# Optimization experiments

Measured on AMD Instinct MI355X. Metric: run time of the kernel, lower is better.

Reference implementation:

```python
import jax, jax.numpy as jnp
import numpy as np

B, C, H, W = 8, 512, 96, 96
CQ = 64  # inter_ch


def setup_inputs() -> dict:
    key = jax.random.key(0)
    ks = jax.random.split(key, 8)
    scale = 1.0 / np.sqrt(C)
    return {
        "x": jax.random.normal(ks[0], (B, C, H, W), dtype=jnp.float32),
        "Wq": jax.random.normal(ks[1], (CQ, C), dtype=jnp.float32) * scale,
        "bq": jax.random.normal(ks[2], (CQ,), dtype=jnp.float32) * 0.01,
        "Wk": jax.random.normal(ks[3], (CQ, C), dtype=jnp.float32) * scale,
        "bk": jax.random.normal(ks[4], (CQ,), dtype=jnp.float32) * 0.01,
        "Wv": jax.random.normal(ks[5], (C, C), dtype=jnp.float32) * scale,
        "bv": jax.random.normal(ks[6], (C,), dtype=jnp.float32) * 0.01,
        "gamma": jax.random.normal(ks[7], (1,), dtype=jnp.float32) * 0.1,
    }


def reference(x, Wq, bq, Wk, bk, Wv, bv, gamma):
    # 1x1 convs expressed as channel matmuls; outputs in BHWC layout
    Q = jnp.einsum('bchw,oc->bhwo', x, Wq) + bq   # [B,H,W,CQ]
    K = jnp.einsum('bchw,oc->bhwo', x, Wk) + bk   # [B,H,W,CQ]
    V = jnp.einsum('bchw,oc->bhwo', x, Wv) + bv   # [B,H,W,C]

    # Per pixel (i,j): keys = concat(row i keys [W], column j keys [H]).
    # NOTE: this replication includes pixel (i,j) twice (once in row, once in col),
    # matching the torch loop exactly (no -INF masking as in original CCNet).
    e_row = jnp.einsum('bhwc,bhvc->bhwv', Q, K)   # [B,H,W,W] attend along row h
    e_col = jnp.einsum('bhwc,bgwc->bhwg', Q, K)   # [B,H,W,H] attend along col w
    attn = jax.nn.softmax(jnp.concatenate([e_row, e_col], axis=-1), axis=-1)
    a_row, a_col = attn[..., :W], attn[..., W:]   # [B,H,W,W], [B,H,W,H]

    out = (jnp.einsum('bhwv,bhvc->bhwc', a_row, V)
           + jnp.einsum('bhwg,bgwc->bhwc', a_col, V))  # [B,H,W,C]
    out = jnp.transpose(out, (0, 3, 1, 2))        # [B,C,H,W]
    return x + gamma[0] * out
```

## Files before the change

### kernel.cpp

```cpp
#include <hip/hip_runtime.h>
#include <stdint.h>

#define B_  8
#define C_  512
#define H_  96
#define W_  96
#define CQ_ 64
#define P_  (H_*W_)
#define NP  (B_*P_)
#define L_  (W_+H_)

typedef __attribute__((ext_vector_type(8))) short short8;
typedef __attribute__((ext_vector_type(4))) float f32x4;
typedef __attribute__((ext_vector_type(4))) unsigned short us4;

__device__ __forceinline__ ushort f2bf(float f) {
    uint32_t u = __builtin_bit_cast(uint32_t, f);
    u += 0x7fff + ((u >> 16) & 1);
    return (ushort)(u >> 16);
}
__device__ __forceinline__ float bf2f(ushort h) {
    uint32_t u = ((uint32_t)h) << 16;
    return __builtin_bit_cast(float, u);
}

#define GLL16(g, l) __builtin_amdgcn_global_load_lds( \
    (const __attribute__((address_space(1))) uint32_t*)(g), \
    (__attribute__((address_space(3))) uint32_t*)(l), 16, 0, 0)

#define FSW(r) (((r) >> 1) & 3)

__global__ __launch_bounds__(256) void k_xt(const float* __restrict__ x, ushort* __restrict__ xt) {
    __shared__ float tile[64][65];
    int p0 = blockIdx.x * 64, c0 = blockIdx.y * 64, bat = blockIdx.z;
    int tx = threadIdx.x, ty = threadIdx.y;
    const float* xb = x + ((size_t)bat * C_ + c0) * P_ + p0;
    #pragma unroll
    for (int i = ty; i < 64; i += 8) {
        float2 v = *(const float2*)&xb[(size_t)i * P_ + 2 * tx];
        tile[i][2 * tx] = v.x; tile[i][2 * tx + 1] = v.y;
    }
    __syncthreads();
    ushort* o = xt + ((size_t)bat * P_ + p0) * C_ + c0;
    #pragma unroll
    for (int i = ty; i < 64; i += 8) {
        ushort2 v; v.x = f2bf(tile[2 * tx][i]); v.y = f2bf(tile[2 * tx + 1][i]);
        *(ushort2*)&o[(size_t)i * C_ + 2 * tx] = v;
    }
}

__global__ __launch_bounds__(256) void k_wconv(const float* __restrict__ Wq, const float* __restrict__ Wk,
                                               const float* __restrict__ Wv, const float* __restrict__ bq,
                                               const float* __restrict__ bk, const float* __restrict__ bv,
                                               ushort* __restrict__ Wall, float* __restrict__ ball) {
    int idx = blockIdx.x * 256 + threadIdx.x;
    if (idx < 640) {
        float b;
        if (idx < 64)       b = bq[idx];
        else if (idx < 128) b = bk[idx - 64];
        else                b = bv[idx - 128];
        ball[idx] = b;
    }
    if (idx >= 640 * C_) return;
    int o = idx / C_, c = idx % C_;
    float v;
    if (o < 64)       v = Wq[o * C_ + c];
    else if (o < 128) v = Wk[(o - 64) * C_ + c];
    else              v = Wv[(o - 128) * C_ + c];
    Wall[idx] = f2bf(v);
}

__global__ __launch_bounds__(256, 4) void k_proj(const ushort* __restrict__ xt, const ushort* __restrict__ Wall,
                                                 const float* __restrict__ ball,
                                                 ushort* __restrict__ Qcm, ushort* __restrict__ Kcm,
                                                 ushort* __restrict__ Vcm) {
    __shared__ __align__(16) ushort Al[128 * 32];
    __shared__ __align__(16) ushort Bl[128 * 32];
    int tid = threadIdx.x, lane = tid & 63, wv = tid >> 6;
    int wr = wv >> 1, wc = wv & 1;
    int wg = ((int)blockIdx.x & 7) * 360 + ((int)blockIdx.x >> 3);
    int m0 = (wg % 5) * 128;
    int n0 = (wg / 5) * 128;
    f32x4 acc[4][4] = {};
    for (int kb = 0; kb < C_; kb += 32) {
        #pragma unroll
        for (int i = 0; i < 2; ++i) {
            int u = tid + i * 256, row = u >> 2, seg = u & 3;
            int sg = (seg ^ FSW(row)) << 3;
            GLL16(&Wall[(size_t)(m0 + row) * C_ + kb + sg], &Al[(size_t)u * 8]);
            GLL16(&xt[(size_t)(n0 + row) * C_ + kb + sg],   &Bl[(size_t)u * 8]);
        }
        __syncthreads();
        int rr = lane & 15, gq = lane >> 4, ck = gq ^ FSW(rr);
        short8 fb[4];
        #pragma unroll
        for (int nt = 0; nt < 4; ++nt) fb[nt] = *(const short8*)&Bl[(wc * 64 + nt * 16 + rr) * 32 + ck * 8];
        #pragma unroll
        for (int mt = 0; mt < 4; ++mt) {
            short8 fa = *(const short8*)&Al[(wr * 64 + mt * 16 + rr) * 32 + ck * 8];
            #pragma unroll
            for (int nt = 0; nt < 4; ++nt)
                acc[mt][nt] = __builtin_amdgcn_mfma_f32_16x16x32_bf16(fa, fb[nt], acc[mt][nt], 0, 0, 0);
        }
        __syncthreads();
    }
    int rr = lane & 15, gq = lane >> 4;
    int bat = n0 / P_, pb0 = n0 - bat * P_;
    #pragma unroll
    for (int mt = 0; mt < 4; ++mt)
        #pragma unroll
        for (int nt = 0; nt < 4; ++nt) {
            int col = wc * 64 + nt * 16 + rr;
            #pragma unroll
            for (int q = 0; q < 4; ++q) {
                int o = m0 + wr * 64 + mt * 16 + gq * 4 + q;
                float v = acc[mt][nt][q] + ball[o];
                if (o < 64)       Qcm[(size_t)o * NP + n0 + col] = f2bf(v);
                else if (o < 128) Kcm[(size_t)(o - 64) * NP + n0 + col] = f2bf(v);
                else              Vcm[((size_t)bat * C_ + (o - 128)) * P_ + pb0 + col] = f2bf(v);
            }
        }
}

__global__ __launch_bounds__(256) void k_qkt(const ushort* __restrict__ Qcm, const ushort* __restrict__ Kcm,
                                             ushort* __restrict__ Qb, ushort* __restrict__ Kb) {
    __shared__ ushort t[64][65];
    int p0 = blockIdx.x * 64;
    const ushort* src = blockIdx.y ? Kcm : Qcm;
    ushort* dst = blockIdx.y ? Kb : Qb;
    int tx = threadIdx.x, ty = threadIdx.y;
    #pragma unroll
    for (int i = ty; i < 64; i += 4) t[i][tx] = src[(size_t)i * NP + p0 + tx];
    __syncthreads();
    #pragma unroll
    for (int i = ty; i < 64; i += 4) dst[(size_t)(p0 + i) * CQ_ + tx] = t[tx][i];
}

__global__ __launch_bounds__(256) void k_vt(const ushort* __restrict__ Vcm, ushort* __restrict__ Vt) {
    __shared__ ushort t[96 * 98];
    int c = blockIdx.x, bat = blockIdx.y;
    const ushort* src = Vcm + ((size_t)(bat * C_ + c)) * P_;
    int tid = threadIdx.x;
    for (int u = tid; u < 2304; u += 256) {
        int h = u / 24, w4 = (u % 24) * 4;
        us4 v = *(const us4*)&src[h * 96 + w4];
        ushort2 a; a.x = v.x; a.y = v.y;
        ushort2 b; b.x = v.z; b.y = v.w;
        *(ushort2*)&t[h * 98 + w4]     = a;
        *(ushort2*)&t[h * 98 + w4 + 2] = b;
    }
    __syncthreads();
    for (int u = tid; u < 2304; u += 256) {
        int w = u / 24, h4 = (u % 24) * 4;
        us4 o;
        o.x = t[(h4 + 0) * 98 + w];
        o.y = t[(h4 + 1) * 98 + w];
        o.z = t[(h4 + 2) * 98 + w];
        o.w = t[(h4 + 3) * 98 + w];
        *(us4*)&Vt[((size_t)(bat * W_ + w) * C_ + c) * H_ + h4] = o;
    }
}

#define LSTR 40
__global__ __launch_bounds__(256) void k_erow(const ushort* __restrict__ Qb, const ushort* __restrict__ Kb,
                                              float* __restrict__ logits) {
    __shared__ __align__(16) ushort Al[96 * LSTR];
    __shared__ __align__(16) ushort Bl[96 * LSTR];
    int h = blockIdx.x, bat = blockIdx.y;
    int tid = threadIdx.x, lane = tid & 63, wvid = tid >> 6;
    int wr = wvid >> 1, wc = wvid & 1;
    size_t base = ((size_t)bat * H_ + h) * W_;
    f32x4 acc[3][3] = {};
    for (int kb = 0; kb < CQ_; kb += 32) {
        for (int s = tid; s < 96 * 4; s += 256) {
            int row = s >> 2, seg = s & 3;
            *(short8*)&Al[row * LSTR + seg * 8] = *(const short8*)&Qb[(base + row) * CQ_ + kb + seg * 8];
            *(short8*)&Bl[row * LSTR + seg * 8] = *(const short8*)&Kb[(base + row) * CQ_ + kb + seg * 8];
        }
        __syncthreads();
        int rr = lane & 15, gq = lane >> 4;
        #pragma unroll
        for (int mt = 0; mt < 3; ++mt) {
            short8 fa = *(const short8*)&Al[(wr * 48 + mt * 16 + rr) * LSTR + gq * 8];
            #pragma unroll
            for (int nt = 0; nt < 3; ++nt) {
                short8 fb = *(const short8*)&Bl[(wc * 48 + nt * 16 + rr) * LSTR + gq * 8];
                acc[mt][nt] = __builtin_amdgcn_mfma_f32_16x16x32_bf16(fa, fb, acc[mt][nt], 0, 0, 0);
            }
        }
        __syncthreads();
    }
    int rr = lane & 15, gq = lane >> 4;
    #pragma unroll
    for (int mt = 0; mt < 3; ++mt)
        #pragma unroll
        for (int nt = 0; nt < 3; ++nt)
            #pragma unroll
            for (int q = 0; q < 4; ++q) {
                int w = wr * 48 + mt * 16 + gq * 4 + q;
                int v = wc * 48 + nt * 16 + rr;
                logits[(base + w) * L_ + v] = acc[mt][nt][q];
            }
}

__global__ __launch_bounds__(256) void k_ecol(const ushort* __restrict__ Qb, const ushort* __restrict__ Kb,
                                              float* __restrict__ logits) {
    __shared__ __align__(16) ushort Al[96 * LSTR];
    __shared__ __align__(16) ushort Bl[96 * LSTR];
    int w = blockIdx.x, bat = blockIdx.y;
    int tid = threadIdx.x, lane = tid & 63, wvid = tid >> 6;
    int wr = wvid >> 1, wc = wvid & 1;
    f32x4 acc[3][3] = {};
    for (int kb = 0; kb < CQ_; kb += 32) {
        for (int s = tid; s < 96 * 4; s += 256) {
            int row = s >> 2, seg = s & 3;
            size_t px = ((size_t)bat * H_ + row) * W_ + w;
            *(short8*)&Al[row * LSTR + seg * 8] = *(const short8*)&Qb[px * CQ_ + kb + seg * 8];
            *(short8*)&Bl[row * LSTR + seg * 8] = *(const short8*)&Kb[px * CQ_ + kb + seg * 8];
        }
        __syncthreads();
        int rr = lane & 15, gq = lane >> 4;
        #pragma unroll
        for (int mt = 0; mt < 3; ++mt) {
            short8 fa = *(const short8*)&Al[(wr * 48 + mt * 16 + rr) * LSTR + gq * 8];
            #pragma unroll
            for (int nt = 0; nt < 3; ++nt) {
                short8 fb = *(const short8*)&Bl[(wc * 48 + nt * 16 + rr) * LSTR + gq * 8];
                acc[mt][nt] = __builtin_amdgcn_mfma_f32_16x16x32_bf16(fa, fb, acc[mt][nt], 0, 0, 0);
            }
        }
        __syncthreads();
    }
    int rr = lane & 15, gq = lane >> 4;
    #pragma unroll
    for (int mt = 0; mt < 3; ++mt)
        #pragma unroll
        for (int nt = 0; nt < 3; ++nt)
            #pragma unroll
            for (int q = 0; q < 4; ++q) {
                int hh = wr * 48 + mt * 16 + gq * 4 + q;
                int gg = wc * 48 + nt * 16 + rr;
                logits[(((size_t)bat * H_ + hh) * W_ + w) * L_ + W_ + gg] = acc[mt][nt][q];
            }
}

__global__ __launch_bounds__(256) void k_softmax(const float* __restrict__ logits, ushort* __restrict__ attn) {
    int wvid = threadIdx.x >> 6, lane = threadIdx.x & 63;
    size_t px = (size_t)blockIdx.x * 4 + wvid;
    const float* lp = logits + px * L_;
    float v0 = lp[lane], v1 = lp[lane + 64], v2 = lp[lane + 128];
    float m = fmaxf(fmaxf(v0, v1), v2);
    #pragma unroll
    for (int off = 32; off; off >>= 1) m = fmaxf(m, __shfl_xor(m, off));
    float e0 = __expf(v0 - m), e1 = __expf(v1 - m), e2 = __expf(v2 - m);
    float s = e0 + e1 + e2;
    #pragma unroll
    for (int off = 32; off; off >>= 1) s += __shfl_xor(s, off);
    float inv = 1.0f / s;
    ushort* ap = attn + px * L_;
    ap[lane] = f2bf(e0 * inv); ap[lane + 64] = f2bf(e1 * inv); ap[lane + 128] = f2bf(e2 * inv);
}

__global__ __launch_bounds__(512) void k_pvcol(const ushort* __restrict__ Vt, const ushort* __restrict__ attn,
                                               ushort* __restrict__ out1t) {
    __shared__ __align__(16) ushort Al[512 * 32];
    __shared__ __align__(16) ushort Bl[96 * 32];
    int w = blockIdx.x, bat = blockIdx.y;
    int tid = threadIdx.x, lane = tid & 63, wvid = tid >> 6;
    int wrm = wvid >> 1, wcn = wvid & 1;
    size_t vbase = ((size_t)bat * W_ + w) * C_ * H_;
    size_t abase = ((size_t)bat * P_ + w) * L_ + W_;
    f32x4 acc[8][3] = {};
    for (int kb = 0; kb < 96; kb += 32) {
        #pragma unroll
        for (int i = 0; i < 4; ++i) {
            int u = tid + i * 512, row = u >> 2, seg = u & 3;
            int sg = (seg ^ FSW(row)) << 3;
            GLL16(&Vt[vbase + (size_t)row * H_ + kb + sg], &Al[(size_t)u * 8]);
        }
        if (tid < 384) {
            int row = tid >> 2, seg = tid & 3;
            int sg = (seg ^ FSW(row)) << 3;
            GLL16(&attn[abase + (size_t)row * (W_ * L_) + kb + sg], &Bl[(size_t)tid * 8]);
        }
        __syncthreads();
        int rr = lane & 15, gq = lane >> 4, ck = gq ^ FSW(rr);
        short8 fb[3];
        #pragma unroll
        for (int nt = 0; nt < 3; ++nt) fb[nt] = *(const short8*)&Bl[(wcn * 48 + nt * 16 + rr) * 32 + ck * 8];
        #pragma unroll
        for (int mt = 0; mt < 8; ++mt) {
            short8 fa = *(const short8*)&Al[(wrm * 128 + mt * 16 + rr) * 32 + ck * 8];
            #pragma unroll
            for (int nt = 0; nt < 3; ++nt)
                acc[mt][nt] = __builtin_amdgcn_mfma_f32_16x16x32_bf16(fa, fb[nt], acc[mt][nt], 0, 0, 0);
        }
        __syncthreads();
    }
    int rr = lane & 15, gq = lane >> 4;
    #pragma unroll
    for (int mt = 0; mt < 8; ++mt)
        #pragma unroll
        for (int nt = 0; nt < 3; ++nt) {
            int hh = wcn * 48 + nt * 16 + rr;
            #pragma unroll
            for (int q = 0; q < 4; ++q) {
                int c = wrm * 128 + mt * 16 + gq * 4 + q;
                out1t[((size_t)(bat * C_ + c) * W_ + w) * H_ + hh] = f2bf(acc[mt][nt][q]);
            }
        }
}

__global__ __launch_bounds__(512) void k_pvrow(const ushort* __restrict__ Vcm, const ushort* __restrict__ attn,
                                               ushort* __restrict__ out0) {
    __shared__ __align__(16) ushort Al[512 * 32];
    __shared__ __align__(16) ushort Bl[96 * 32];
    int h = blockIdx.x, bat = blockIdx.y;
    int tid = threadIdx.x, lane = tid & 63, wvid = tid >> 6;
    int wrm = wvid >> 1, wcn = wvid & 1;
    size_t vbase = (size_t)bat * C_ * P_ + (size_t)h * W_;
    size_t abase = ((size_t)bat * H_ + h) * W_ * L_;
    f32x4 acc[8][3] = {};
    for (int kb = 0; kb < 96; kb += 32) {
        #pragma unroll
        for (int i = 0; i < 4; ++i) {
            int u = tid + i * 512, row = u >> 2, seg = u & 3;
            int sg = (seg ^ FSW(row)) << 3;
            GLL16(&Vcm[vbase + (size_t)row * P_ + kb + sg], &Al[(size_t)u * 8]);
        }
        if (tid < 384) {
            int row = tid >> 2, seg = tid & 3;
            int sg = (seg ^ FSW(row)) << 3;
            GLL16(&attn[abase + (size_t)row * L_ + kb + sg], &Bl[(size_t)tid * 8]);
        }
        __syncthreads();
        int rr = lane & 15, gq = lane >> 4, ck = gq ^ FSW(rr);
        short8 fb[3];
        #pragma unroll
        for (int nt = 0; nt < 3; ++nt) fb[nt] = *(const short8*)&Bl[(wcn * 48 + nt * 16 + rr) * 32 + ck * 8];
        #pragma unroll
        for (int mt = 0; mt < 8; ++mt) {
            short8 fa = *(const short8*)&Al[(wrm * 128 + mt * 16 + rr) * 32 + ck * 8];
            #pragma unroll
            for (int nt = 0; nt < 3; ++nt)
                acc[mt][nt] = __builtin_amdgcn_mfma_f32_16x16x32_bf16(fa, fb[nt], acc[mt][nt], 0, 0, 0);
        }
        __syncthreads();
    }
    int rr = lane & 15, gq = lane >> 4;
    #pragma unroll
    for (int mt = 0; mt < 8; ++mt)
        #pragma unroll
        for (int nt = 0; nt < 3; ++nt) {
            int w = wcn * 48 + nt * 16 + rr;
            #pragma unroll
            for (int q = 0; q < 4; ++q) {
                int c = wrm * 128 + mt * 16 + gq * 4 + q;
                out0[((size_t)bat * C_ + c) * P_ + (size_t)h * W_ + w] = f2bf(acc[mt][nt][q]);
            }
        }
}

__global__ __launch_bounds__(256) void k_final(const float* __restrict__ x, const ushort* __restrict__ out0,
                                               const ushort* __restrict__ out1t, const float* __restrict__ gamma,
                                               float* __restrict__ out) {
    __shared__ ushort t[96 * 98];
    int c = blockIdx.x, bat = blockIdx.y;
    const ushort* src = out1t + ((size_t)bat * C_ + c) * P_;
    int tid = threadIdx.x;
    for (int i = tid; i < 4608; i += 256) {
        int w = i / 48, h = (i % 48) * 2;
        ushort2 v = *(const ushort2*)&src[w * 96 + h];
        *(ushort2*)&t[w * 98 + h] = v;
    }
    __syncthreads();
    float gm = gamma[0];
    size_t base = ((size_t)bat * C_ + c) * P_;
    for (int i = tid; i < 4608; i += 256) {
        int h = i / 48, w = (i % 48) * 2;
        size_t idx = base + h * W_ + w;
        float2 xv = *(const float2*)&x[idx];
        ushort2 o0 = *(const ushort2*)&out0[idx];
        float2 r;
        r.x = xv.x + gm * (bf2f(o0.x) + bf2f(t[w * 98 + h]));
        r.y = xv.y + gm * (bf2f(o0.y) + bf2f(t[(w + 1) * 98 + h]));
        *(float2*)&out[idx] = r;
    }
}

extern "C" void kernel_launch(void* const* d_in, const int* in_sizes, int n_in,
                              void* d_out, int out_size, void* d_ws, size_t ws_size,
                              hipStream_t stream) {
    const float* x     = (const float*)d_in[0];
    const float* Wq    = (const float*)d_in[1];
    const float* bq    = (const float*)d_in[2];
    const float* Wk    = (const float*)d_in[3];
    const float* bk    = (const float*)d_in[4];
    const float* Wv    = (const float*)d_in[5];
    const float* bv    = (const float*)d_in[6];
    const float* gamma = (const float*)d_in[7];
    float* out = (float*)d_out;
    char* ws = (char*)d_ws;

    const size_t SZ  = (size_t)NP * C_ * 2;
    const size_t QKS = (size_t)NP * CQ_ * 2;
    ushort* xt     = (ushort*)(ws);
    ushort* out1t  = (ushort*)(ws);
    ushort* Vcm    = (ushort*)(ws + SZ);
    ushort* Vt     = (ushort*)(ws + 2 * SZ);
    ushort* out0   = Vt;
    ushort* Qcm    = (ushort*)(ws + 3 * SZ);
    ushort* Kcm    = (ushort*)(ws + 3 * SZ + QKS);
    float*  logits = (float*) (ws + 3 * SZ + 2 * QKS);
    ushort* Qb     = (ushort*)(ws + 4 * SZ);
    ushort* Kb     = (ushort*)(ws + 4 * SZ + QKS);
    ushort* attn   = (ushort*)(ws + 4 * SZ);
    size_t off_wall = 4 * SZ + (size_t)NP * L_ * 2;
    ushort* Wall   = (ushort*)(ws + off_wall);
    float*  ball   = (float*) (ws + off_wall + 640 * C_ * 2);

    k_wconv  <<<dim3(1280),       dim3(256),   0, stream>>>(Wq, Wk, Wv, bq, bk, bv, Wall, ball);
    k_xt     <<<dim3(144, 8, 8),  dim3(32, 8), 0, stream>>>(x, xt);
    k_proj   <<<dim3(2880),       dim3(256),   0, stream>>>(xt, Wall, ball, Qcm, Kcm, Vcm);
    k_qkt    <<<dim3(1152, 2),    dim3(64, 4), 0, stream>>>(Qcm, Kcm, Qb, Kb);
    k_vt     <<<dim3(512, 8),     dim3(256),   0, stream>>>(Vcm, Vt);
    k_erow   <<<dim3(96, 8),      dim3(256),   0, stream>>>(Qb, Kb, logits);
    k_ecol   <<<dim3(96, 8),      dim3(256),   0, stream>>>(Qb, Kb, logits);
    k_softmax<<<dim3(NP / 4),     dim3(256),   0, stream>>>(logits, attn);
    k_pvcol  <<<dim3(96, 8),      dim3(512),   0, stream>>>(Vt, attn, out1t);
    k_pvrow  <<<dim3(96, 8),      dim3(512),   0, stream>>>(Vcm, attn, out0);
    k_final  <<<dim3(512, 8),     dim3(256),   0, stream>>>(x, out0, out1t, gamma, out);
}
```

Measured before the change: 394.0 us.

## Fuse Q/K transpose into projection epilogue and softmax into column-energy kernel

The projection kernel now writes Q and K directly in pixel-major layout via an LDS transpose in its epilogue, which removes the separate k_qkt transpose kernel and the channel-major Q/K buffers. Row energies are stored as bf16 straight into the attention buffer. The column-energy kernel keeps its tile in LDS and performs the full 192-wide softmax per pixel, reading the row logits back, so the fp32 logits buffer and the standalone softmax kernel are gone. This cuts two launches and a large fp32 round trip, at the cost of rounding logits to bf16 before the softmax and running a less parallel softmax loop inside the column kernel.

Measured after the change: 363.0 us. 1.09x faster.

```diff
diff --git a/kernel.cpp b/kernel.cpp
--- a/kernel.cpp
+++ b/kernel.cpp
@@ -72,10 +72,11 @@
 
 __global__ __launch_bounds__(256, 4) void k_proj(const ushort* __restrict__ xt, const ushort* __restrict__ Wall,
                                                  const float* __restrict__ ball,
-                                                 ushort* __restrict__ Qcm, ushort* __restrict__ Kcm,
+                                                 ushort* __restrict__ Qb, ushort* __restrict__ Kb,
                                                  ushort* __restrict__ Vcm) {
     __shared__ __align__(16) ushort Al[128 * 32];
     __shared__ __align__(16) ushort Bl[128 * 32];
+    __shared__ __align__(16) ushort Tl[128 * 68];
     int tid = threadIdx.x, lane = tid & 63, wv = tid >> 6;
     int wr = wv >> 1, wc = wv & 1;
     int wg = ((int)blockIdx.x & 7) * 360 + ((int)blockIdx.x >> 3);
@@ -106,34 +107,44 @@
     }
     int rr = lane & 15, gq = lane >> 4;
     int bat = n0 / P_, pb0 = n0 - bat * P_;
-    #pragma unroll
-    for (int mt = 0; mt < 4; ++mt)
-        #pragma unroll
-        for (int nt = 0; nt < 4; ++nt) {
-            int col = wc * 64 + nt * 16 + rr;
-            #pragma unroll
-            for (int q = 0; q < 4; ++q) {
-                int o = m0 + wr * 64 + mt * 16 + gq * 4 + q;
-                float v = acc[mt][nt][q] + ball[o];
-                if (o < 64)       Qcm[(size_t)o * NP + n0 + col] = f2bf(v);
-                else if (o < 128) Kcm[(size_t)(o - 64) * NP + n0 + col] = f2bf(v);
-                else              Vcm[((size_t)bat * C_ + (o - 128)) * P_ + pb0 + col] = f2bf(v);
-            }
-        }
-}
-
-__global__ __launch_bounds__(256) void k_qkt(const ushort* __restrict__ Qcm, const ushort* __restrict__ Kcm,
-                                             ushort* __restrict__ Qb, ushort* __restrict__ Kb) {
-    __shared__ ushort t[64][65];
-    int p0 = blockIdx.x * 64;
-    const ushort* src = blockIdx.y ? Kcm : Qcm;
-    ushort* dst = blockIdx.y ? Kb : Qb;
-    int tx = threadIdx.x, ty = threadIdx.y;
-    #pragma unroll
-    for (int i = ty; i < 64; i += 4) t[i][tx] = src[(size_t)i * NP + p0 + tx];
-    __syncthreads();
-    #pragma unroll
-    for (int i = ty; i < 64; i += 4) dst[(size_t)(p0 + i) * CQ_ + tx] = t[tx][i];
+    if (m0 == 0) {
+        #pragma unroll
+        for (int pass = 0; pass < 2; ++pass) {
+            __syncthreads();
+            if (wr == pass) {
+                #pragma unroll
+                for (int mt = 0; mt < 4; ++mt)
+                    #pragma unroll
+                    for (int nt = 0; nt < 4; ++nt) {
+                        int col = wc * 64 + nt * 16 + rr;
+                        #pragma unroll
+                        for (int q = 0; q < 4; ++q) {
+                            int ol = mt * 16 + gq * 4 + q;
+                            Tl[col * 68 + ol] = f2bf(acc[mt][nt][q] + ball[pass * 64 + ol]);
+                        }
+                    }
+            }
+            __syncthreads();
+            ushort* dst = pass ? Kb : Qb;
+            int p = tid >> 1, off = (tid & 1) * 32;
+            #pragma unroll
+            for (int j = 0; j < 8; ++j)
+                *(us4*)&dst[(size_t)(n0 + p) * CQ_ + off + j * 4] = *(const us4*)&Tl[p * 68 + off + j * 4];
+        }
+    } else {
+        #pragma unroll
+        for (int mt = 0; mt < 4; ++mt)
+            #pragma unroll
+            for (int nt = 0; nt < 4; ++nt) {
+                int col = wc * 64 + nt * 16 + rr;
+                #pragma unroll
+                for (int q = 0; q < 4; ++q) {
+                    int o = m0 + wr * 64 + mt * 16 + gq * 4 + q;
+                    int c = o - 128;
+                    Vcm[((size_t)bat * C_ + c) * P_ + pb0 + col] = f2bf(acc[mt][nt][q] + ball[o]);
+                }
+            }
+    }
 }
 
 __global__ __launch_bounds__(256) void k_vt(const ushort* __restrict__ Vcm, ushort* __restrict__ Vt) {
@@ -163,7 +174,7 @@
 
 #define LSTR 40
 __global__ __launch_bounds__(256) void k_erow(const ushort* __restrict__ Qb, const ushort* __restrict__ Kb,
-                                              float* __restrict__ logits) {
+                                              ushort* __restrict__ attn) {
     __shared__ __align__(16) ushort Al[96 * LSTR];
     __shared__ __align__(16) ushort Bl[96 * LSTR];
     int h = blockIdx.x, bat = blockIdx.y;
@@ -199,14 +210,15 @@
             for (int q = 0; q < 4; ++q) {
                 int w = wr * 48 + mt * 16 + gq * 4 + q;
                 int v = wc * 48 + nt * 16 + rr;
-                logits[(base + w) * L_ + v] = acc[mt][nt][q];
-            }
-}
-
-__global__ __launch_bounds__(256) void k_ecol(const ushort* __restrict__ Qb, const ushort* __restrict__ Kb,
-                                              float* __restrict__ logits) {
+                attn[(base + w) * L_ + v] = f2bf(acc[mt][nt][q]);
+            }
+}
+
+__global__ __launch_bounds__(256) void k_ecolsm(const ushort* __restrict__ Qb, const ushort* __restrict__ Kb,
+                                                ushort* __restrict__ attn) {
     __shared__ __align__(16) ushort Al[96 * LSTR];
     __shared__ __align__(16) ushort Bl[96 * LSTR];
+    __shared__ ushort ecl[96 * 100];
     int w = blockIdx.x, bat = blockIdx.y;
     int tid = threadIdx.x, lane = tid & 63, wvid = tid >> 6;
     int wr = wvid >> 1, wc = wvid & 1;
@@ -231,34 +243,43 @@
         }
         __syncthreads();
     }
-    int rr = lane & 15, gq = lane >> 4;
-    #pragma unroll
-    for (int mt = 0; mt < 3; ++mt)
-        #pragma unroll
-        for (int nt = 0; nt < 3; ++nt)
-            #pragma unroll
-            for (int q = 0; q < 4; ++q) {
-                int hh = wr * 48 + mt * 16 + gq * 4 + q;
-                int gg = wc * 48 + nt * 16 + rr;
-                logits[(((size_t)bat * H_ + hh) * W_ + w) * L_ + W_ + gg] = acc[mt][nt][q];
-            }
-}
-
-__global__ __launch_bounds__(256) void k_softmax(const float* __restrict__ logits, ushort* __restrict__ attn) {
-    int wvid = threadIdx.x >> 6, lane = threadIdx.x & 63;
-    size_t px = (size_t)blockIdx.x * 4 + wvid;
-    const float* lp = logits + px * L_;
-    float v0 = lp[lane], v1 = lp[lane + 64], v2 = lp[lane + 128];
-    float m = fmaxf(fmaxf(v0, v1), v2);
-    #pragma unroll
-    for (int off = 32; off; off >>= 1) m = fmaxf(m, __shfl_xor(m, off));
-    float e0 = __expf(v0 - m), e1 = __expf(v1 - m), e2 = __expf(v2 - m);
-    float s = e0 + e1 + e2;
-    #pragma unroll
-    for (int off = 32; off; off >>= 1) s += __shfl_xor(s, off);
-    float inv = 1.0f / s;
-    ushort* ap = attn + px * L_;
-    ap[lane] = f2bf(e0 * inv); ap[lane + 64] = f2bf(e1 * inv); ap[lane + 128] = f2bf(e2 * inv);
+    {
+        int rr = lane & 15, gq = lane >> 4;
+        #pragma unroll
+        for (int mt = 0; mt < 3; ++mt)
+            #pragma unroll
+            for (int nt = 0; nt < 3; ++nt)
+                #pragma unroll
+                for (int q = 0; q < 4; ++q) {
+                    int hh = wr * 48 + mt * 16 + gq * 4 + q;
+                    int gg = wc * 48 + nt * 16 + rr;
+                    ecl[hh * 100 + gg] = f2bf(acc[mt][nt][q]);
+                }
+    }
+    __syncthreads();
+    for (int h = wvid; h < H_; h += 4) {
+        size_t pix = ((size_t)bat * H_ + h) * W_ + w;
+        ushort* ap = attn + pix * L_;
+        float a  = bf2f(ap[lane]);
+        float b  = (lane < 32) ? bf2f(ap[64 + lane]) : -1e30f;
+        float c0 = bf2f(ecl[h * 100 + lane]);
+        float c1 = (lane < 32) ? bf2f(ecl[h * 100 + 64 + lane]) : -1e30f;
+        float m = fmaxf(fmaxf(a, b), fmaxf(c0, c1));
+        #pragma unroll
+        for (int off = 32; off; off >>= 1) m = fmaxf(m, __shfl_xor(m, off));
+        float ea = __expf(a - m), eb = (lane < 32) ? __expf(b - m) : 0.0f;
+        float ec0 = __expf(c0 - m), ec1 = (lane < 32) ? __expf(c1 - m) : 0.0f;
+        float s = ea + eb + ec0 + ec1;
+        #pragma unroll
+        for (int off = 32; off; off >>= 1) s += __shfl_xor(s, off);
+        float inv = 1.0f / s;
+        ap[lane] = f2bf(ea * inv);
+        ap[96 + lane] = f2bf(ec0 * inv);
+        if (lane < 32) {
+            ap[64 + lane] = f2bf(eb * inv);
+            ap[160 + lane] = f2bf(ec1 * inv);
+        }
+    }
 }
 
 __global__ __launch_bounds__(512) void k_pvcol(const ushort* __restrict__ Vt, const ushort* __restrict__ attn,
@@ -409,24 +430,19 @@
     ushort* Vcm    = (ushort*)(ws + SZ);
     ushort* Vt     = (ushort*)(ws + 2 * SZ);
     ushort* out0   = Vt;
-    ushort* Qcm    = (ushort*)(ws + 3 * SZ);
-    ushort* Kcm    = (ushort*)(ws + 3 * SZ + QKS);
-    float*  logits = (float*) (ws + 3 * SZ + 2 * QKS);
-    ushort* Qb     = (ushort*)(ws + 4 * SZ);
-    ushort* Kb     = (ushort*)(ws + 4 * SZ + QKS);
-    ushort* attn   = (ushort*)(ws + 4 * SZ);
-    size_t off_wall = 4 * SZ + (size_t)NP * L_ * 2;
+    ushort* Qb     = (ushort*)(ws + 3 * SZ);
+    ushort* Kb     = (ushort*)(ws + 3 * SZ + QKS);
+    ushort* attn   = (ushort*)(ws + 3 * SZ + 2 * QKS);
+    size_t off_wall = 3 * SZ + 2 * QKS + (size_t)NP * L_ * 2;
     ushort* Wall   = (ushort*)(ws + off_wall);
     float*  ball   = (float*) (ws + off_wall + 640 * C_ * 2);
 
     k_wconv  <<<dim3(1280),       dim3(256),   0, stream>>>(Wq, Wk, Wv, bq, bk, bv, Wall, ball);
     k_xt     <<<dim3(144, 8, 8),  dim3(32, 8), 0, stream>>>(x, xt);
-    k_proj   <<<dim3(2880),       dim3(256),   0, stream>>>(xt, Wall, ball, Qcm, Kcm, Vcm);
-    k_qkt    <<<dim3(1152, 2),    dim3(64, 4), 0, stream>>>(Qcm, Kcm, Qb, Kb);
+    k_proj   <<<dim3(2880),       dim3(256),   0, stream>>>(xt, Wall, ball, Qb, Kb, Vcm);
     k_vt     <<<dim3(512, 8),     dim3(256),   0, stream>>>(Vcm, Vt);
-    k_erow   <<<dim3(96, 8),      dim3(256),   0, stream>>>(Qb, Kb, logits);
-    k_ecol   <<<dim3(96, 8),      dim3(256),   0, stream>>>(Qb, Kb, logits);
-    k_softmax<<<dim3(NP / 4),     dim3(256),   0, stream>>>(logits, attn);
+    k_erow   <<<dim3(96, 8),      dim3(256),   0, stream>>>(Qb, Kb, attn);
+    k_ecolsm <<<dim3(96, 8),      dim3(256),   0, stream>>>(Qb, Kb, attn);
     k_pvcol  <<<dim3(96, 8),      dim3(512),   0, stream>>>(Vt, attn, out1t);
     k_pvrow  <<<dim3(96, 8),      dim3(512),   0, stream>>>(Vcm, attn, out0);
     k_final  <<<dim3(512, 8),     dim3(256),   0, stream>>>(x, out0, out1t, gamma, out);
```
